# Kernel tuning notes

Hardware: AMD Instinct MI355X
Metric: run time of the kernel (lower is better)

## Reference

```python
import jax, jax.numpy as jnp
import numpy as np

BANDWIDTH = 1.0
EPS = 1e-20


def setup_inputs() -> dict:
    key = jax.random.key(0)
    k1, k2, k3 = jax.random.split(key, 3)
    test_X = jax.random.normal(k1, (8192, 64), dtype=jnp.float32)
    train_X = jax.random.normal(k2, (16384, 64), dtype=jnp.float32)
    sample_weight = jax.random.uniform(k3, (16384,), dtype=jnp.float32)
    return {"test_X": test_X, "train_X": train_X, "sample_weight": sample_weight}


def reference(test_X, train_X, sample_weight):
    # test_X: [m, d], train_X: [n, d], sample_weight: [n]
    d = train_X.shape[1]
    h = jnp.float32(BANDWIDTH)
    # weights are normalized; with weights, n is treated as 1 => log(n) = 0
    w = sample_weight / jnp.sum(sample_weight)
    Z = 0.5 * d * jnp.log(2.0 * jnp.float32(np.pi)) + d * jnp.log(h)
    # squared L2 distances via expansion (avoids [m, n, d] intermediate)
    t2 = jnp.sum(test_X * test_X, axis=-1)  # [m]
    r2 = jnp.sum(train_X * train_X, axis=-1)  # [n]
    cross = test_X @ train_X.T  # [m, n]
    sq = (t2[:, None] + r2[None, :] - 2.0 * cross) / (h * h)  # [m, n]
    val = -0.5 * sq - Z  # [m, n]
    # weighted, numerically-stable log-sum-exp over train dim
    m_max = jnp.max(val, axis=-1, keepdims=True)  # [m, 1]
    s = jnp.sum(jnp.exp(val - m_max) * w[None, :], axis=-1)  # [m]
    return m_max[:, 0] + jnp.log(s + EPS)
```

## Files before the change

### kernel.cpp

```cpp
#include <hip/hip_runtime.h>
#include <hip/hip_bf16.h>
#include <math.h>

#define M 8192
#define N 16384
#define D 64
#define ZC 58.81206612509905f
#define B0 24.0f
#define LOG2E 1.4426950408889634f
#define HL2E 0.7213475204444817f
#define LN2 0.6931471805599453f

#define SCH_K 8388608.0f
#define SCH_C (1065353216.0f - 0.0435f * 8388608.0f)

#define PCH 16
#define NCHK (N / PCH)

typedef short v8bf __attribute__((ext_vector_type(8)));
typedef float v16f __attribute__((ext_vector_type(16)));

#define B_AU2  0
#define B_LW2  32768
#define B_PART 98304
#define B_TB   622592
#define B_TR   1671168

__global__ __launch_bounds__(256) void gk_prep(const float* __restrict__ testX,
                                               const float* __restrict__ trainX,
                                               const float* __restrict__ sw,
                                               __hip_bfloat16* __restrict__ tb,
                                               __hip_bfloat16* __restrict__ rb,
                                               float* __restrict__ au2,
                                               float* __restrict__ lw2) {
    const int tid = threadIdx.x;
    const int e = tid & 7;
    if (blockIdx.x < M / 32) {
        const int row = blockIdx.x * 32 + (tid >> 3);
        const float4* p = reinterpret_cast<const float4*>(testX + (size_t)row * D + e * 8);
        float4 v0 = p[0], v1 = p[1];
        float t2 = v0.x * v0.x + v0.y * v0.y + v0.z * v0.z + v0.w * v0.w
                 + v1.x * v1.x + v1.y * v1.y + v1.z * v1.z + v1.w * v1.w;
        t2 += __shfl_xor(t2, 1, 64);
        t2 += __shfl_xor(t2, 2, 64);
        t2 += __shfl_xor(t2, 4, 64);
        if (e == 0) au2[row] = -HL2E * t2;
        union { __hip_bfloat16 h[8]; uint4 u; } cv;
        cv.h[0] = __float2bfloat16(v0.x * LOG2E);
        cv.h[1] = __float2bfloat16(v0.y * LOG2E);
        cv.h[2] = __float2bfloat16(v0.z * LOG2E);
        cv.h[3] = __float2bfloat16(v0.w * LOG2E);
        cv.h[4] = __float2bfloat16(v1.x * LOG2E);
        cv.h[5] = __float2bfloat16(v1.y * LOG2E);
        cv.h[6] = __float2bfloat16(v1.z * LOG2E);
        cv.h[7] = __float2bfloat16(v1.w * LOG2E);
        *reinterpret_cast<uint4*>(tb + (size_t)row * D + e * 8) = cv.u;
    } else {
        const int row = (blockIdx.x - M / 32) * 32 + (tid >> 3);
        const float4* p = reinterpret_cast<const float4*>(trainX + (size_t)row * D + e * 8);
        float4 v0 = p[0], v1 = p[1];
        float r2 = v0.x * v0.x + v0.y * v0.y + v0.z * v0.z + v0.w * v0.w
                 + v1.x * v1.x + v1.y * v1.y + v1.z * v1.z + v1.w * v1.w;
        r2 += __shfl_xor(r2, 1, 64);
        r2 += __shfl_xor(r2, 2, 64);
        r2 += __shfl_xor(r2, 4, 64);
        if (e == 0) lw2[row] = __builtin_amdgcn_logf(sw[row]) - HL2E * r2 + B0;
        union { __hip_bfloat16 h[8]; uint4 u; } cv;
        cv.h[0] = __float2bfloat16(v0.x);
        cv.h[1] = __float2bfloat16(v0.y);
        cv.h[2] = __float2bfloat16(v0.z);
        cv.h[3] = __float2bfloat16(v0.w);
        cv.h[4] = __float2bfloat16(v1.x);
        cv.h[5] = __float2bfloat16(v1.y);
        cv.h[6] = __float2bfloat16(v1.z);
        cv.h[7] = __float2bfloat16(v1.w);
        *reinterpret_cast<uint4*>(rb + (size_t)row * D + e * 8) = cv.u;
    }
}

__device__ __forceinline__ void dma16(const void* g, void* l) {
    __builtin_amdgcn_global_load_lds(
        (const __attribute__((address_space(1))) unsigned int*)g,
        (__attribute__((address_space(3))) unsigned int*)l, 16, 0, 0);
}

__device__ __forceinline__ void dma_tile(const __hip_bfloat16* tr, int nt,
                                         char* Bsb, int w, int lane) {
#pragma unroll
    for (int i = 0; i < 2; ++i) {
        const int g = w * 2 + i;
        const __hip_bfloat16* gp =
            tr + (size_t)(nt + g * 8 + (lane & 7)) * D + (lane >> 3) * 8;
        dma16(gp, Bsb + g * 1024);
    }
}

__device__ __forceinline__ void compute_tile(const char* Bs, float lwa, float lwb,
                                             const v8bf af[4], const v16f& zacc,
                                             float srun[16], int c, int h) {
#pragma unroll
    for (int s = 0; s < 2; ++s) {
        const float cs = fmaf(s ? lwb : lwa, SCH_K, SCH_C);
        const v8bf bf0 = *reinterpret_cast<const v8bf*>(
            Bs + (s * 4 + (c >> 3)) * 1024 + (0 + h) * 128 + (c & 7) * 16);
        v16f acc = __builtin_amdgcn_mfma_f32_32x32x16_bf16(af[0], bf0, zacc, 0, 0, 0);
#pragma unroll
        for (int t = 1; t < 4; ++t) {
            const v8bf bf = *reinterpret_cast<const v8bf*>(
                Bs + (s * 4 + (c >> 3)) * 1024 + (2 * t + h) * 128 + (c & 7) * 16);
            acc = __builtin_amdgcn_mfma_f32_32x32x16_bf16(af[t], bf, acc, 0, 0, 0);
        }
#pragma unroll
        for (int r = 0; r < 16; ++r) {
            float tv = fmaf(acc[r], SCH_K, cs);
            tv = fmaxf(tv, 0.0f);
            srun[r] += __int_as_float((int)tv);
        }
    }
}

__global__ __launch_bounds__(256, 4) void gk_main(const __hip_bfloat16* __restrict__ ta,
                                                  const __hip_bfloat16* __restrict__ tr,
                                                  const float* __restrict__ lw2,
                                                  float* __restrict__ part) {
    __shared__ __align__(16) char smem[24576];
    const int tid = threadIdx.x;
    const int w = tid >> 6;
    const int lane = tid & 63;
    const int c = lane & 31;
    const int h = lane >> 5;

    const int bid = blockIdx.x;
    const int xcd = bid & 7;
    const int j = bid >> 3;
    const int chunk = xcd * 2 + (j & 1);
    const int m0 = (j >> 1) * 128;
    const int n0 = chunk * NCHK;

    char* const Bs[3] = { smem, smem + 8192, smem + 16384 };

    float lwa[3], lwb[3];

    dma_tile(tr, n0, Bs[0], w, lane);
    lwa[0] = lw2[n0 + c]; lwb[0] = lw2[n0 + 32 + c];

    const __hip_bfloat16* arow = ta + (size_t)(m0 + w * 32 + c) * D;
    v8bf af[4];
#pragma unroll
    for (int t = 0; t < 4; ++t)
        af[t] = *reinterpret_cast<const v8bf*>(arow + (2 * t + h) * 8);

    dma_tile(tr, n0 + 64, Bs[1], w, lane);
    lwa[1] = lw2[n0 + 64 + c]; lwb[1] = lw2[n0 + 96 + c];

    v16f zacc;
#pragma unroll
    for (int r = 0; r < 16; ++r) zacc[r] = 0.f;
    float srun[16];
#pragma unroll
    for (int r = 0; r < 16; ++r) srun[r] = 0.f;

#pragma unroll
    for (int t = 0; t < 16; ++t) {
        if (t < 15) {
            asm volatile("s_waitcnt vmcnt(4)" ::: "memory");
        } else {
            asm volatile("s_waitcnt vmcnt(0)" ::: "memory");
        }
        __builtin_amdgcn_s_barrier();
        if (t + 2 < 16) {
            dma_tile(tr, n0 + (t + 2) * 64, Bs[(t + 2) % 3], w, lane);
            lwa[(t + 2) % 3] = lw2[n0 + (t + 2) * 64 + c];
            lwb[(t + 2) % 3] = lw2[n0 + (t + 2) * 64 + 32 + c];
        }
        compute_tile(Bs[t % 3], lwa[t % 3], lwb[t % 3], af, zacc, srun, c, h);
    }

    __syncthreads();
    float* red = reinterpret_cast<float*>(smem);
#pragma unroll
    for (int r = 0; r < 16; ++r) {
        int rowl = (r & 3) + 8 * (r >> 2) + 4 * h;
        red[(w * 32 + rowl) * 33 + c] = srun[r];
    }
    __syncthreads();
    if (tid < 128) {
        float G = 0.f;
#pragma unroll
        for (int c2 = 0; c2 < 32; ++c2) G += red[tid * 33 + c2];
        part[(size_t)chunk * M + m0 + tid] = G;
    }
}

__global__ __launch_bounds__(256) void gk_merge(const float* __restrict__ part,
                                                const float* __restrict__ au2,
                                                const float* __restrict__ sw,
                                                float* __restrict__ out) {
    __shared__ float red[256];
    const int tid = threadIdx.x;
    float s = 0.f;
    const float4* p4 = reinterpret_cast<const float4*>(sw);
    for (int i = tid; i < N / 4; i += 256) {
        float4 v = p4[i];
        s += v.x + v.y + v.z + v.w;
    }
    red[tid] = s;
    __syncthreads();
    for (int off = 128; off > 0; off >>= 1) {
        if (tid < off) red[tid] += red[tid + off];
        __syncthreads();
    }
    const float W = red[0];

    const int r = blockIdx.x * 256 + tid;
    float G = 0.f;
#pragma unroll
    for (int p = 0; p < PCH; ++p) G += part[(size_t)p * M + r];
    out[r] = LN2 * (au2[r] + __builtin_amdgcn_logf(fmaxf(G, 1e-30f)) - B0
                   - __builtin_amdgcn_logf(W)) - ZC;
}

extern "C" void kernel_launch(void* const* d_in, const int* in_sizes, int n_in,
                              void* d_out, int out_size, void* d_ws, size_t ws_size,
                              hipStream_t stream) {
    const float* testX  = (const float*)d_in[0];
    const float* trainX = (const float*)d_in[1];
    const float* sw     = (const float*)d_in[2];
    float* out = (float*)d_out;
    char* wsb = (char*)d_ws;

    float* au2  = (float*)(wsb + B_AU2);
    float* lw2  = (float*)(wsb + B_LW2);
    float* part = (float*)(wsb + B_PART);
    __hip_bfloat16* tb = (__hip_bfloat16*)(wsb + B_TB);
    __hip_bfloat16* rb = (__hip_bfloat16*)(wsb + B_TR);

    gk_prep<<<M / 32 + N / 32, 256, 0, stream>>>(testX, trainX, sw, tb, rb, au2, lw2);
    gk_main<<<(M / 128) * PCH, 256, 0, stream>>>(tb, rb, lw2, part);
    gk_merge<<<M / 256, 256, 0, stream>>>(part, au2, sw, out);
}
```

Before: 92.96 us.

## Load train tiles directly from global memory instead of LDS triple buffering

Removes the global-to-LDS DMA triple-buffer pipeline with its per-tile barriers and waitcnts. Each wave now reads its B fragments straight from global memory (relying on L1/L2 caching), since all four waves share the same train rows. This drops barrier synchronisation and LDS traffic, frees LDS for occupancy, and leans on the cache plus compiler scheduling to hide load latency. In exchange there is redundant global/L2 traffic across waves and a risk of exposed memory latency.

Measured after the change: 128.5 us. 1.38x slower.

```diff
diff --git a/kernel.cpp b/kernel.cpp
--- a/kernel.cpp
+++ b/kernel.cpp
@@ -78,52 +78,11 @@
     }
 }
 
-__device__ __forceinline__ void dma16(const void* g, void* l) {
-    __builtin_amdgcn_global_load_lds(
-        (const __attribute__((address_space(1))) unsigned int*)g,
-        (__attribute__((address_space(3))) unsigned int*)l, 16, 0, 0);
-}
-
-__device__ __forceinline__ void dma_tile(const __hip_bfloat16* tr, int nt,
-                                         char* Bsb, int w, int lane) {
-#pragma unroll
-    for (int i = 0; i < 2; ++i) {
-        const int g = w * 2 + i;
-        const __hip_bfloat16* gp =
-            tr + (size_t)(nt + g * 8 + (lane & 7)) * D + (lane >> 3) * 8;
-        dma16(gp, Bsb + g * 1024);
-    }
-}
-
-__device__ __forceinline__ void compute_tile(const char* Bs, float lwa, float lwb,
-                                             const v8bf af[4], const v16f& zacc,
-                                             float srun[16], int c, int h) {
-#pragma unroll
-    for (int s = 0; s < 2; ++s) {
-        const float cs = fmaf(s ? lwb : lwa, SCH_K, SCH_C);
-        const v8bf bf0 = *reinterpret_cast<const v8bf*>(
-            Bs + (s * 4 + (c >> 3)) * 1024 + (0 + h) * 128 + (c & 7) * 16);
-        v16f acc = __builtin_amdgcn_mfma_f32_32x32x16_bf16(af[0], bf0, zacc, 0, 0, 0);
-#pragma unroll
-        for (int t = 1; t < 4; ++t) {
-            const v8bf bf = *reinterpret_cast<const v8bf*>(
-                Bs + (s * 4 + (c >> 3)) * 1024 + (2 * t + h) * 128 + (c & 7) * 16);
-            acc = __builtin_amdgcn_mfma_f32_32x32x16_bf16(af[t], bf, acc, 0, 0, 0);
-        }
-#pragma unroll
-        for (int r = 0; r < 16; ++r) {
-            float tv = fmaf(acc[r], SCH_K, cs);
-            tv = fmaxf(tv, 0.0f);
-            srun[r] += __int_as_float((int)tv);
-        }
-    }
-}
-
 __global__ __launch_bounds__(256, 4) void gk_main(const __hip_bfloat16* __restrict__ ta,
                                                   const __hip_bfloat16* __restrict__ tr,
                                                   const float* __restrict__ lw2,
                                                   float* __restrict__ part) {
-    __shared__ __align__(16) char smem[24576];
+    __shared__ __align__(16) float red[128 * 33];
     const int tid = threadIdx.x;
     const int w = tid >> 6;
     const int lane = tid & 63;
@@ -137,21 +96,11 @@
     const int m0 = (j >> 1) * 128;
     const int n0 = chunk * NCHK;
 
-    char* const Bs[3] = { smem, smem + 8192, smem + 16384 };
-
-    float lwa[3], lwb[3];
-
-    dma_tile(tr, n0, Bs[0], w, lane);
-    lwa[0] = lw2[n0 + c]; lwb[0] = lw2[n0 + 32 + c];
-
     const __hip_bfloat16* arow = ta + (size_t)(m0 + w * 32 + c) * D;
     v8bf af[4];
 #pragma unroll
     for (int t = 0; t < 4; ++t)
         af[t] = *reinterpret_cast<const v8bf*>(arow + (2 * t + h) * 8);
-
-    dma_tile(tr, n0 + 64, Bs[1], w, lane);
-    lwa[1] = lw2[n0 + 64 + c]; lwb[1] = lw2[n0 + 96 + c];
 
     v16f zacc;
 #pragma unroll
@@ -160,24 +109,31 @@
 #pragma unroll
     for (int r = 0; r < 16; ++r) srun[r] = 0.f;
 
+    const __hip_bfloat16* bp0 = tr + (size_t)(n0 + c) * D + h * 8;
+    const float* lwp = lw2 + n0 + c;
+
+#pragma unroll 2
+    for (int t = 0; t < 16; ++t) {
 #pragma unroll
-    for (int t = 0; t < 16; ++t) {
-        if (t < 15) {
-            asm volatile("s_waitcnt vmcnt(4)" ::: "memory");
-        } else {
-            asm volatile("s_waitcnt vmcnt(0)" ::: "memory");
+        for (int s = 0; s < 2; ++s) {
+            const float lwv = lwp[t * 64 + s * 32];
+            const float cs = fmaf(lwv, SCH_K, SCH_C);
+            const __hip_bfloat16* bp = bp0 + (size_t)(t * 64 + s * 32) * D;
+            v16f acc = __builtin_amdgcn_mfma_f32_32x32x16_bf16(
+                af[0], *reinterpret_cast<const v8bf*>(bp), zacc, 0, 0, 0);
+#pragma unroll
+            for (int q = 1; q < 4; ++q)
+                acc = __builtin_amdgcn_mfma_f32_32x32x16_bf16(
+                    af[q], *reinterpret_cast<const v8bf*>(bp + q * 16), acc, 0, 0, 0);
+#pragma unroll
+            for (int r = 0; r < 16; ++r) {
+                float tv = fmaf(acc[r], SCH_K, cs);
+                tv = fmaxf(tv, 0.0f);
+                srun[r] += __int_as_float((int)tv);
+            }
         }
-        __builtin_amdgcn_s_barrier();
-        if (t + 2 < 16) {
-            dma_tile(tr, n0 + (t + 2) * 64, Bs[(t + 2) % 3], w, lane);
-            lwa[(t + 2) % 3] = lw2[n0 + (t + 2) * 64 + c];
-            lwb[(t + 2) % 3] = lw2[n0 + (t + 2) * 64 + 32 + c];
-        }
-        compute_tile(Bs[t % 3], lwa[t % 3], lwb[t % 3], af, zacc, srun, c, h);
     }
 
-    __syncthreads();
-    float* red = reinterpret_cast<float*>(smem);
 #pragma unroll
     for (int r = 0; r < 16; ++r) {
         int rowl = (r & 3) + 8 * (r >> 2) + 4 * h;
```
